# Kernel optimization log

Hardware: AMD Instinct MI355X
Metric: run time of the kernel (lower is better)

The kernel has to match this reference:

```python
import jax, jax.numpy as jnp
import numpy as np

LN_EPS = 1e-5
LEAKY_SLOPE = 0.01

N_NODES = 50000
N_EDGES = 800000
NODE_DIM = 128
EDGE_DIM = 128
CAT_DIM = EDGE_DIM + 2 * NODE_DIM  # 384


def setup_inputs() -> dict:
    key = jax.random.key(0)
    ks = jax.random.split(key, 6)
    node_feat = jax.random.normal(ks[0], (N_NODES, NODE_DIM), dtype=jnp.float32)
    edge_src = jax.random.randint(ks[1], (N_EDGES,), 0, N_NODES, dtype=jnp.int64)
    edge_dst = jax.random.randint(ks[2], (N_EDGES,), 0, N_NODES, dtype=jnp.int64)
    e = jax.random.normal(ks[3], (N_EDGES, EDGE_DIM), dtype=jnp.float32)
    ln_gamma = jnp.ones((CAT_DIM,), dtype=jnp.float32)
    ln_beta = jnp.zeros((CAT_DIM,), dtype=jnp.float32)
    # Linear weights stored as [in, out]; scaled like torch default init
    W1 = jax.random.normal(ks[4], (CAT_DIM, EDGE_DIM), dtype=jnp.float32) / np.sqrt(CAT_DIM)
    b1 = jnp.zeros((EDGE_DIM,), dtype=jnp.float32)
    W2 = jax.random.normal(ks[5], (EDGE_DIM, EDGE_DIM), dtype=jnp.float32) / np.sqrt(EDGE_DIM)
    b2 = jnp.zeros((EDGE_DIM,), dtype=jnp.float32)
    return {"node_feat": node_feat, "edge_src": edge_src, "edge_dst": edge_dst,
            "e": e, "ln_gamma": ln_gamma, "ln_beta": ln_beta,
            "W1": W1, "b1": b1, "W2": W2, "b2": b2}


def reference(node_feat, edge_src, edge_dst, e, ln_gamma, ln_beta, W1, b1, W2, b2):
    # gather endpoint node features per edge: [E, node_dim] each
    x_i = node_feat[edge_src]
    x_j = node_feat[edge_dst]
    cat = jnp.concatenate([x_i, x_j, e], axis=-1)  # [E, cat_dim]
    # LayerNorm over last dim
    mu = jnp.mean(cat, axis=-1, keepdims=True)
    var = jnp.mean(jnp.square(cat - mu), axis=-1, keepdims=True)
    z = (cat - mu) * jax.lax.rsqrt(var + LN_EPS) * ln_gamma + ln_beta
    # Linear -> LeakyReLU -> Linear (dropout=0)
    h1 = z @ W1 + b1
    h1 = jnp.where(h1 >= 0, h1, LEAKY_SLOPE * h1)
    h2 = h1 @ W2 + b2
    # residual update of edge features
    return e + h2
```

## Files before the change

### kernel.cpp

```cpp
#include <hip/hip_runtime.h>
#include <hip/hip_bf16.h>

typedef __attribute__((ext_vector_type(8))) short short8;
typedef __attribute__((ext_vector_type(4))) float f32x4;

#define NEDGES 800000
#define BM 32
#define NTILES (NEDGES / BM)
#define CAT 384
#define APAD 8
#define STRIDE (CAT + APAD)
#define GRIDSZ 512

__device__ __forceinline__ unsigned short f2bf(float f) {
  union { float f; unsigned u; } v; v.f = f;
  unsigned r = v.u + 0x7fffu + ((v.u >> 16) & 1u);
  return (unsigned short)(r >> 16);
}

__device__ __forceinline__ float bf2f(unsigned short u) {
  union { unsigned u; float f; } v; v.u = ((unsigned)u) << 16;
  return v.f;
}


__global__ void prep_w(const float* __restrict__ W1, const float* __restrict__ gamma,
                       const float* __restrict__ W2,
                       unsigned short* __restrict__ Wgt, unsigned short* __restrict__ W2t) {
  int idx = blockIdx.x * 256 + threadIdx.x;
  if (idx < 128 * 384) {
    int n = idx / 384, k = idx % 384;
    Wgt[idx] = f2bf(gamma[k] * W1[k * 128 + n]);
  }
  if (idx < 128 * 128) {
    int n = idx / 128, k = idx % 128;
    W2t[idx] = f2bf(W2[k * 128 + n]);
  }
}

__global__ void prep_gc(const float* __restrict__ W1, const float* __restrict__ gamma,
                        const float* __restrict__ beta, const float* __restrict__ b1,
                        float* __restrict__ G, float* __restrict__ C1) {
  int n = threadIdx.x;
  float g = 0.f, b = 0.f;
  for (int k = 0; k < 384; ++k) {
    float w = W1[k * 128 + n];
    g = fmaf(gamma[k], w, g);
    b = fmaf(beta[k], w, b);
  }
  G[n] = g;
  C1[n] = b + b1[n];
}

__global__ __launch_bounds__(256, 2) void edge_fused(
    const float* __restrict__ node_feat,
    const int* __restrict__ esrc,
    const int* __restrict__ edst,
    const float* __restrict__ eptr,
    const unsigned short* __restrict__ Wgt,
    const unsigned short* __restrict__ W2t,
    const float* __restrict__ Gv,
    const float* __restrict__ C1v,
    const float* __restrict__ b2v,
    float* __restrict__ out) {
  __shared__ unsigned short Abuf[2][BM][STRIDE];
  __shared__ float muS[2][BM];
  __shared__ float rsS[2][BM];

  const int tid = threadIdx.x;
  const int r  = tid >> 3;
  const int tt = tid & 7;
  const int l = tid & 63;
  const int w = tid >> 6;
  const int lr = l & 15;
  const int lkrow = l >> 4;
  const int lk = lkrow * 8;
  const int n0 = w * 32;

  short8 B1[2][12];
  short8 B2[2][4];
  float Gn[2], C1n[2];
  float4 b2q[2];
#pragma unroll
  for (int nf = 0; nf < 2; ++nf) {
    const int n = n0 + nf * 16 + lr;
    Gn[nf] = Gv[n]; C1n[nf] = C1v[n];
    b2q[nf] = *(const float4*)&b2v[n0 + nf * 16 + lkrow * 4];
#pragma unroll
    for (int ks = 0; ks < 12; ++ks)
      B1[nf][ks] = *(const short8*)&Wgt[(size_t)n * CAT + ks * 32 + lk];
#pragma unroll
    for (int ks = 0; ks < 4; ++ks)
      B2[nf][ks] = *(const short8*)&W2t[(size_t)n * 128 + ks * 32 + lk];
  }

  float4 ev[4], xi[4], xj[4];
  int siP, diP;

  auto stage = [&](int q) {
    float sum = 0.f, sq = 0.f;
#pragma unroll
    for (int i = 0; i < 4; ++i) {
      float4 v = ev[i];
      sum += (v.x + v.y) + (v.z + v.w);
      sq = fmaf(v.x, v.x, sq); sq = fmaf(v.y, v.y, sq);
      sq = fmaf(v.z, v.z, sq); sq = fmaf(v.w, v.w, sq);
      ushort4 pk; pk.x = f2bf(v.x); pk.y = f2bf(v.y); pk.z = f2bf(v.z); pk.w = f2bf(v.w);
      *(ushort4*)&Abuf[q][r][256 + (tt + 8 * i) * 4] = pk;
    }
#pragma unroll
    for (int i = 0; i < 4; ++i) {
      float4 v = xi[i];
      sum += (v.x + v.y) + (v.z + v.w);
      sq = fmaf(v.x, v.x, sq); sq = fmaf(v.y, v.y, sq);
      sq = fmaf(v.z, v.z, sq); sq = fmaf(v.w, v.w, sq);
      ushort4 pk; pk.x = f2bf(v.x); pk.y = f2bf(v.y); pk.z = f2bf(v.z); pk.w = f2bf(v.w);
      *(ushort4*)&Abuf[q][r][0 + (tt + 8 * i) * 4] = pk;
    }
#pragma unroll
    for (int i = 0; i < 4; ++i) {
      float4 v = xj[i];
      sum += (v.x + v.y) + (v.z + v.w);
      sq = fmaf(v.x, v.x, sq); sq = fmaf(v.y, v.y, sq);
      sq = fmaf(v.z, v.z, sq); sq = fmaf(v.w, v.w, sq);
      ushort4 pk; pk.x = f2bf(v.x); pk.y = f2bf(v.y); pk.z = f2bf(v.z); pk.w = f2bf(v.w);
      *(ushort4*)&Abuf[q][r][128 + (tt + 8 * i) * 4] = pk;
    }
    sum += __shfl_xor(sum, 1); sum += __shfl_xor(sum, 2); sum += __shfl_xor(sum, 4);
    sq  += __shfl_xor(sq, 1);  sq  += __shfl_xor(sq, 2);  sq  += __shfl_xor(sq, 4);
    const float mu = sum * (1.f / 384.f);
    const float var = fmaf(-mu, mu, sq * (1.f / 384.f));
    const float rstd = rsqrtf(var + 1e-5f);
    if (tt == 0) { muS[q][r] = mu; rsS[q][r] = rstd; }
  };

  auto gather = [&](int tl) {
    const size_t g = (size_t)tl * BM + r;
    const float4* __restrict__ pe = (const float4*)(eptr + g * 128);
    const float4* __restrict__ pi = (const float4*)(node_feat + (size_t)siP * 128);
    const float4* __restrict__ pj = (const float4*)(node_feat + (size_t)diP * 128);
#pragma unroll
    for (int i = 0; i < 4; ++i) ev[i] = pe[tt + 8 * i];
#pragma unroll
    for (int i = 0; i < 4; ++i) xi[i] = pi[tt + 8 * i];
#pragma unroll
    for (int i = 0; i < 4; ++i) xj[i] = pj[tt + 8 * i];
  };

  int tile = blockIdx.x;
  {
    const size_t g0 = (size_t)tile * BM + r;
    siP = esrc[g0]; diP = edst[g0];
    gather(tile);
  }
  int tnext = tile + GRIDSZ;
  if (tnext < NTILES) {
    const size_t g1 = (size_t)tnext * BM + r;
    siP = esrc[g1]; diP = edst[g1];
  }
  stage(0);
  if (tnext < NTILES) {
    gather(tnext);
    const int t3 = tnext + GRIDSZ;
    if (t3 < NTILES) {
      const size_t g3 = (size_t)t3 * BM + r;
      siP = esrc[g3]; diP = edst[g3];
    }
  }
  __syncthreads();

  int p = 0;
  for (;;) {
    f32x4 acc[2][2];
#pragma unroll
    for (int mf = 0; mf < 2; ++mf)
#pragma unroll
      for (int nf = 0; nf < 2; ++nf)
        acc[mf][nf] = (f32x4){0.f, 0.f, 0.f, 0.f};
#pragma unroll
    for (int ks = 0; ks < 12; ++ks) {
      short8 af0 = *(const short8*)&Abuf[p][lr][ks * 32 + lk];
      short8 af1 = *(const short8*)&Abuf[p][16 + lr][ks * 32 + lk];
      acc[0][0] = __builtin_amdgcn_mfma_f32_16x16x32_bf16(af0, B1[0][ks], acc[0][0], 0, 0, 0);
      acc[0][1] = __builtin_amdgcn_mfma_f32_16x16x32_bf16(af0, B1[1][ks], acc[0][1], 0, 0, 0);
      acc[1][0] = __builtin_amdgcn_mfma_f32_16x16x32_bf16(af1, B1[0][ks], acc[1][0], 0, 0, 0);
      acc[1][1] = __builtin_amdgcn_mfma_f32_16x16x32_bf16(af1, B1[1][ks], acc[1][1], 0, 0, 0);
    }
    __syncthreads();

#pragma unroll
    for (int mf = 0; mf < 2; ++mf) {
#pragma unroll
      for (int nf = 0; nf < 2; ++nf) {
        const int n = n0 + nf * 16 + lr;
#pragma unroll
        for (int j = 0; j < 4; ++j) {
          const int m = mf * 16 + lkrow * 4 + j;
          float h = fmaf(rsS[p][m], acc[mf][nf][j] - muS[p][m] * Gn[nf], C1n[nf]);
          h = (h >= 0.f) ? h : 0.01f * h;
          Abuf[p][m][n] = f2bf(h);
        }
      }
    }
    __syncthreads();

    f32x4 acc2[2][2];
#pragma unroll
    for (int mf = 0; mf < 2; ++mf)
#pragma unroll
      for (int nf = 0; nf < 2; ++nf)
        acc2[mf][nf] = (f32x4){0.f, 0.f, 0.f, 0.f};
#pragma unroll
    for (int ks = 0; ks < 4; ++ks) {
      short8 h0 = *(const short8*)&Abuf[p][lr][ks * 32 + lk];
      short8 h1 = *(const short8*)&Abuf[p][16 + lr][ks * 32 + lk];
      acc2[0][0] = __builtin_amdgcn_mfma_f32_16x16x32_bf16(B2[0][ks], h0, acc2[0][0], 0, 0, 0);
      acc2[0][1] = __builtin_amdgcn_mfma_f32_16x16x32_bf16(B2[1][ks], h0, acc2[0][1], 0, 0, 0);
      acc2[1][0] = __builtin_amdgcn_mfma_f32_16x16x32_bf16(B2[0][ks], h1, acc2[1][0], 0, 0, 0);
      acc2[1][1] = __builtin_amdgcn_mfma_f32_16x16x32_bf16(B2[1][ks], h1, acc2[1][1], 0, 0, 0);
    }

    const size_t base = (size_t)tile * BM * 128;
#pragma unroll
    for (int mf = 0; mf < 2; ++mf) {
      const int m = mf * 16 + lr;
#pragma unroll
      for (int nf = 0; nf < 2; ++nf) {
        const int nb = n0 + nf * 16 + lkrow * 4;
        ushort4 e4 = *(const ushort4*)&Abuf[p][m][256 + nb];
        float4 o;
        o.x = bf2f(e4.x) + acc2[mf][nf][0] + b2q[nf].x;
        o.y = bf2f(e4.y) + acc2[mf][nf][1] + b2q[nf].y;
        o.z = bf2f(e4.z) + acc2[mf][nf][2] + b2q[nf].z;
        o.w = bf2f(e4.w) + acc2[mf][nf][3] + b2q[nf].w;
        *(float4*)&out[base + (size_t)m * 128 + nb] = o;
      }
    }

    if (tnext >= NTILES) break;

    stage(p ^ 1);

    const int t3 = tnext + GRIDSZ;
    if (t3 < NTILES) {
      gather(t3);
      const int t4 = t3 + GRIDSZ;
      if (t4 < NTILES) {
        const size_t g4 = (size_t)t4 * BM + r;
        siP = esrc[g4]; diP = edst[g4];
      }
    }
    __syncthreads();
    p ^= 1;
    tile = tnext;
    tnext = t3;
  }
}

extern "C" void kernel_launch(void* const* d_in, const int* in_sizes, int n_in,
                              void* d_out, int out_size, void* d_ws, size_t ws_size,
                              hipStream_t stream) {
  const float* node_feat = (const float*)d_in[0];
  const int* esrc        = (const int*)d_in[1];
  const int* edst        = (const int*)d_in[2];
  const float* e         = (const float*)d_in[3];
  const float* gamma     = (const float*)d_in[4];
  const float* beta      = (const float*)d_in[5];
  const float* W1        = (const float*)d_in[6];
  const float* b1        = (const float*)d_in[7];
  const float* W2        = (const float*)d_in[8];
  const float* b2        = (const float*)d_in[9];
  float* out = (float*)d_out;

  unsigned short* Wgt = (unsigned short*)d_ws;
  unsigned short* W2t = Wgt + 128 * 384;
  float* G  = (float*)(W2t + 128 * 128);
  float* C1 = G + 128;

  prep_w<<<192, 256, 0, stream>>>(W1, gamma, W2, Wgt, W2t);
  prep_gc<<<1, 128, 0, stream>>>(W1, gamma, beta, b1, G, C1);

  edge_fused<<<GRIDSZ, 256, 0, stream>>>(node_feat, esrc, edst, e,
                                         Wgt, W2t, G, C1, b2, out);
}
```

Baseline: 270.7 us.

## Use 512-thread blocks with 16-column wave tiles and transposed first MFMA

Doubles the block to 512 threads (8 waves), so each wave owns 16 output columns instead of 32, and each row is gathered by 16 threads instead of 8. The first GEMM swaps its MFMA operands so the accumulator layout matches the second GEMM, which lets the LeakyReLU result be written as packed ushort4 instead of scalar stores. Per-thread register use for weights and gathered data is halved to reach higher occupancy and more memory parallelism. In exchange there are more waves per block competing at the barriers, and the A fragments in shared memory are read redundantly across more waves.

```diff
diff --git a/kernel.cpp b/kernel.cpp
--- a/kernel.cpp
+++ b/kernel.cpp
@@ -52,7 +52,7 @@
   C1[n] = b + b1[n];
 }
 
-__global__ __launch_bounds__(256, 2) void edge_fused(
+__global__ __launch_bounds__(512, 4) void edge_fused(
     const float* __restrict__ node_feat,
     const int* __restrict__ esrc,
     const int* __restrict__ edst,
@@ -68,66 +68,63 @@
   __shared__ float rsS[2][BM];
 
   const int tid = threadIdx.x;
-  const int r  = tid >> 3;
-  const int tt = tid & 7;
-  const int l = tid & 63;
-  const int w = tid >> 6;
+  const int r  = tid >> 4;
+  const int tt = tid & 15;
+  const int l  = tid & 63;
+  const int wv = tid >> 6;
   const int lr = l & 15;
   const int lkrow = l >> 4;
   const int lk = lkrow * 8;
-  const int n0 = w * 32;
-
-  short8 B1[2][12];
-  short8 B2[2][4];
-  float Gn[2], C1n[2];
-  float4 b2q[2];
-#pragma unroll
-  for (int nf = 0; nf < 2; ++nf) {
-    const int n = n0 + nf * 16 + lr;
-    Gn[nf] = Gv[n]; C1n[nf] = C1v[n];
-    b2q[nf] = *(const float4*)&b2v[n0 + nf * 16 + lkrow * 4];
-#pragma unroll
-    for (int ks = 0; ks < 12; ++ks)
-      B1[nf][ks] = *(const short8*)&Wgt[(size_t)n * CAT + ks * 32 + lk];
-#pragma unroll
-    for (int ks = 0; ks < 4; ++ks)
-      B2[nf][ks] = *(const short8*)&W2t[(size_t)n * 128 + ks * 32 + lk];
-  }
-
-  float4 ev[4], xi[4], xj[4];
+  const int n0 = wv * 16;
+
+  short8 B1[12];
+  short8 B2[4];
+#pragma unroll
+  for (int ks = 0; ks < 12; ++ks)
+    B1[ks] = *(const short8*)&Wgt[(size_t)(n0 + lr) * CAT + ks * 32 + lk];
+#pragma unroll
+  for (int ks = 0; ks < 4; ++ks)
+    B2[ks] = *(const short8*)&W2t[(size_t)(n0 + lr) * 128 + ks * 32 + lk];
+  const float4 Gq  = *(const float4*)&Gv[n0 + lkrow * 4];
+  const float4 C1q = *(const float4*)&C1v[n0 + lkrow * 4];
+  const float4 b2q = *(const float4*)&b2v[n0 + lkrow * 4];
+
+  float4 ev[2], xi[2], xj[2];
   int siP, diP;
 
   auto stage = [&](int q) {
     float sum = 0.f, sq = 0.f;
 #pragma unroll
-    for (int i = 0; i < 4; ++i) {
+    for (int i = 0; i < 2; ++i) {
       float4 v = ev[i];
       sum += (v.x + v.y) + (v.z + v.w);
       sq = fmaf(v.x, v.x, sq); sq = fmaf(v.y, v.y, sq);
       sq = fmaf(v.z, v.z, sq); sq = fmaf(v.w, v.w, sq);
       ushort4 pk; pk.x = f2bf(v.x); pk.y = f2bf(v.y); pk.z = f2bf(v.z); pk.w = f2bf(v.w);
-      *(ushort4*)&Abuf[q][r][256 + (tt + 8 * i) * 4] = pk;
-    }
-#pragma unroll
-    for (int i = 0; i < 4; ++i) {
+      *(ushort4*)&Abuf[q][r][256 + (tt + 16 * i) * 4] = pk;
+    }
+#pragma unroll
+    for (int i = 0; i < 2; ++i) {
       float4 v = xi[i];
       sum += (v.x + v.y) + (v.z + v.w);
       sq = fmaf(v.x, v.x, sq); sq = fmaf(v.y, v.y, sq);
       sq = fmaf(v.z, v.z, sq); sq = fmaf(v.w, v.w, sq);
       ushort4 pk; pk.x = f2bf(v.x); pk.y = f2bf(v.y); pk.z = f2bf(v.z); pk.w = f2bf(v.w);
-      *(ushort4*)&Abuf[q][r][0 + (tt + 8 * i) * 4] = pk;
-    }
-#pragma unroll
-    for (int i = 0; i < 4; ++i) {
+      *(ushort4*)&Abuf[q][r][0 + (tt + 16 * i) * 4] = pk;
+    }
+#pragma unroll
+    for (int i = 0; i < 2; ++i) {
       float4 v = xj[i];
       sum += (v.x + v.y) + (v.z + v.w);
       sq = fmaf(v.x, v.x, sq); sq = fmaf(v.y, v.y, sq);
       sq = fmaf(v.z, v.z, sq); sq = fmaf(v.w, v.w, sq);
       ushort4 pk; pk.x = f2bf(v.x); pk.y = f2bf(v.y); pk.z = f2bf(v.z); pk.w = f2bf(v.w);
-      *(ushort4*)&Abuf[q][r][128 + (tt + 8 * i) * 4] = pk;
-    }
-    sum += __shfl_xor(sum, 1); sum += __shfl_xor(sum, 2); sum += __shfl_xor(sum, 4);
-    sq  += __shfl_xor(sq, 1);  sq  += __shfl_xor(sq, 2);  sq  += __shfl_xor(sq, 4);
+      *(ushort4*)&Abuf[q][r][128 + (tt + 16 * i) * 4] = pk;
+    }
+    sum += __shfl_xor(sum, 1); sum += __shfl_xor(sum, 2);
+    sum += __shfl_xor(sum, 4); sum += __shfl_xor(sum, 8);
+    sq  += __shfl_xor(sq, 1);  sq  += __shfl_xor(sq, 2);
+    sq  += __shfl_xor(sq, 4);  sq  += __shfl_xor(sq, 8);
     const float mu = sum * (1.f / 384.f);
     const float var = fmaf(-mu, mu, sq * (1.f / 384.f));
     const float rstd = rsqrtf(var + 1e-5f);
@@ -139,12 +136,9 @@
     const float4* __restrict__ pe = (const float4*)(eptr + g * 128);
     const float4* __restrict__ pi = (const float4*)(node_feat + (size_t)siP * 128);
     const float4* __restrict__ pj = (const float4*)(node_feat + (size_t)diP * 128);
-#pragma unroll
-    for (int i = 0; i < 4; ++i) ev[i] = pe[tt + 8 * i];
-#pragma unroll
-    for (int i = 0; i < 4; ++i) xi[i] = pi[tt + 8 * i];
-#pragma unroll
-    for (int i = 0; i < 4; ++i) xj[i] = pj[tt + 8 * i];
+    ev[0] = pe[tt]; ev[1] = pe[tt + 16];
+    xi[0] = pi[tt]; xi[1] = pi[tt + 16];
+    xj[0] = pj[tt]; xj[1] = pj[tt + 16];
   };
 
   int tile = blockIdx.x;
@@ -171,70 +165,59 @@
 
   int p = 0;
   for (;;) {
-    f32x4 acc[2][2];
-#pragma unroll
-    for (int mf = 0; mf < 2; ++mf)
-#pragma unroll
-      for (int nf = 0; nf < 2; ++nf)
-        acc[mf][nf] = (f32x4){0.f, 0.f, 0.f, 0.f};
+    f32x4 acc[2];
+    acc[0] = (f32x4){0.f, 0.f, 0.f, 0.f};
+    acc[1] = (f32x4){0.f, 0.f, 0.f, 0.f};
 #pragma unroll
     for (int ks = 0; ks < 12; ++ks) {
       short8 af0 = *(const short8*)&Abuf[p][lr][ks * 32 + lk];
       short8 af1 = *(const short8*)&Abuf[p][16 + lr][ks * 32 + lk];
-      acc[0][0] = __builtin_amdgcn_mfma_f32_16x16x32_bf16(af0, B1[0][ks], acc[0][0], 0, 0, 0);
-      acc[0][1] = __builtin_amdgcn_mfma_f32_16x16x32_bf16(af0, B1[1][ks], acc[0][1], 0, 0, 0);
-      acc[1][0] = __builtin_amdgcn_mfma_f32_16x16x32_bf16(af1, B1[0][ks], acc[1][0], 0, 0, 0);
-      acc[1][1] = __builtin_amdgcn_mfma_f32_16x16x32_bf16(af1, B1[1][ks], acc[1][1], 0, 0, 0);
+      acc[0] = __builtin_amdgcn_mfma_f32_16x16x32_bf16(B1[ks], af0, acc[0], 0, 0, 0);
+      acc[1] = __builtin_amdgcn_mfma_f32_16x16x32_bf16(B1[ks], af1, acc[1], 0, 0, 0);
     }
     __syncthreads();
 
 #pragma unroll
     for (int mf = 0; mf < 2; ++mf) {
-#pragma unroll
-      for (int nf = 0; nf < 2; ++nf) {
-        const int n = n0 + nf * 16 + lr;
-#pragma unroll
-        for (int j = 0; j < 4; ++j) {
-          const int m = mf * 16 + lkrow * 4 + j;
-          float h = fmaf(rsS[p][m], acc[mf][nf][j] - muS[p][m] * Gn[nf], C1n[nf]);
-          h = (h >= 0.f) ? h : 0.01f * h;
-          Abuf[p][m][n] = f2bf(h);
-        }
-      }
+      const int m = lr + 16 * mf;
+      const float mu = muS[p][m];
+      const float rs = rsS[p][m];
+      float h0 = fmaf(rs, acc[mf][0] - mu * Gq.x, C1q.x);
+      float h1 = fmaf(rs, acc[mf][1] - mu * Gq.y, C1q.y);
+      float h2 = fmaf(rs, acc[mf][2] - mu * Gq.z, C1q.z);
+      float h3 = fmaf(rs, acc[mf][3] - mu * Gq.w, C1q.w);
+      h0 = (h0 >= 0.f) ? h0 : 0.01f * h0;
+      h1 = (h1 >= 0.f) ? h1 : 0.01f * h1;
+      h2 = (h2 >= 0.f) ? h2 : 0.01f * h2;
+      h3 = (h3 >= 0.f) ? h3 : 0.01f * h3;
+      ushort4 pk; pk.x = f2bf(h0); pk.y = f2bf(h1); pk.z = f2bf(h2); pk.w = f2bf(h3);
+      *(ushort4*)&Abuf[p][m][n0 + lkrow * 4] = pk;
     }
     __syncthreads();
 
-    f32x4 acc2[2][2];
-#pragma unroll
-    for (int mf = 0; mf < 2; ++mf)
-#pragma unroll
-      for (int nf = 0; nf < 2; ++nf)
-        acc2[mf][nf] = (f32x4){0.f, 0.f, 0.f, 0.f};
+    f32x4 acc2[2];
+    acc2[0] = (f32x4){0.f, 0.f, 0.f, 0.f};
+    acc2[1] = (f32x4){0.f, 0.f, 0.f, 0.f};
 #pragma unroll
     for (int ks = 0; ks < 4; ++ks) {
       short8 h0 = *(const short8*)&Abuf[p][lr][ks * 32 + lk];
       short8 h1 = *(const short8*)&Abuf[p][16 + lr][ks * 32 + lk];
-      acc2[0][0] = __builtin_amdgcn_mfma_f32_16x16x32_bf16(B2[0][ks], h0, acc2[0][0], 0, 0, 0);
-      acc2[0][1] = __builtin_amdgcn_mfma_f32_16x16x32_bf16(B2[1][ks], h0, acc2[0][1], 0, 0, 0);
-      acc2[1][0] = __builtin_amdgcn_mfma_f32_16x16x32_bf16(B2[0][ks], h1, acc2[1][0], 0, 0, 0);
-      acc2[1][1] = __builtin_amdgcn_mfma_f32_16x16x32_bf16(B2[1][ks], h1, acc2[1][1], 0, 0, 0);
+      acc2[0] = __builtin_amdgcn_mfma_f32_16x16x32_bf16(B2[ks], h0, acc2[0], 0, 0, 0);
+      acc2[1] = __builtin_amdgcn_mfma_f32_16x16x32_bf16(B2[ks], h1, acc2[1], 0, 0, 0);
     }
 
     const size_t base = (size_t)tile * BM * 128;
+    const int nb = n0 + lkrow * 4;
 #pragma unroll
     for (int mf = 0; mf < 2; ++mf) {
-      const int m = mf * 16 + lr;
-#pragma unroll
-      for (int nf = 0; nf < 2; ++nf) {
-        const int nb = n0 + nf * 16 + lkrow * 4;
-        ushort4 e4 = *(const ushort4*)&Abuf[p][m][256 + nb];
-        float4 o;
-        o.x = bf2f(e4.x) + acc2[mf][nf][0] + b2q[nf].x;
-        o.y = bf2f(e4.y) + acc2[mf][nf][1] + b2q[nf].y;
-        o.z = bf2f(e4.z) + acc2[mf][nf][2] + b2q[nf].z;
-        o.w = bf2f(e4.w) + acc2[mf][nf][3] + b2q[nf].w;
-        *(float4*)&out[base + (size_t)m * 128 + nb] = o;
-      }
+      const int m = lr + 16 * mf;
+      ushort4 e4 = *(const ushort4*)&Abuf[p][m][256 + nb];
+      float4 o;
+      o.x = bf2f(e4.x) + acc2[mf][0] + b2q.x;
+      o.y = bf2f(e4.y) + acc2[mf][1] + b2q.y;
+      o.z = bf2f(e4.z) + acc2[mf][2] + b2q.z;
+      o.w = bf2f(e4.w) + acc2[mf][3] + b2q.w;
+      *(float4*)&out[base + (size_t)m * 128 + nb] = o;
     }
 
     if (tnext >= NTILES) break;
@@ -280,6 +263,6 @@
   prep_w<<<192, 256, 0, stream>>>(W1, gamma, W2, Wgt, W2t);
   prep_gc<<<1, 128, 0, stream>>>(W1, gamma, beta, b1, G, C1);
 
-  edge_fused<<<GRIDSZ, 256, 0, stream>>>(node_feat, esrc, edst, e,
+  edge_fused<<<GRIDSZ, 512, 0, stream>>>(node_feat, esrc, edst, e,
                                          Wgt, W2t, G, C1, b2, out);
 }
```

Result: slower. 464.4 us (+71.5%).
